# Performance work log

Measured on AMD Instinct MI355X. Metric: run time of the kernel, lower is better.

Reference implementation:

```python
import jax, jax.numpy as jnp
import numpy as np

B = 65536
IN_F = 512
OUT_F = 256
NUM_GROUPS = 8
EPS = 1e-5


def setup_inputs() -> dict:
    key = jax.random.key(0)
    ks = jax.random.split(key, 6)
    return {
        "x": jax.random.normal(ks[0], (B, IN_F), dtype=jnp.float32),
        "weight": jax.random.normal(ks[1], (OUT_F, IN_F), dtype=jnp.float32) * 0.05,
        "bias_linear": jax.random.normal(ks[2], (OUT_F,), dtype=jnp.float32) * 0.05,
        "weight_gn": jax.random.normal(ks[3], (OUT_F,), dtype=jnp.float32),
        "bias_gn": jax.random.normal(ks[4], (OUT_F,), dtype=jnp.float32),
        "bias": jax.random.normal(ks[5], (1, OUT_F, 1, 1), dtype=jnp.float32),
    }


def reference(x, weight, bias_linear, weight_gn, bias_gn, bias):
    # Linear: (B, IN_F) @ (IN_F, OUT_F) + bias -> (B, OUT_F)
    h = jnp.einsum("bi,oi->bo", x, weight) + bias_linear
    # GroupNorm over channel dim (dim=1) with NUM_GROUPS groups
    g = h.reshape(B, NUM_GROUPS, OUT_F // NUM_GROUPS)
    mean = jnp.mean(g, axis=2, keepdims=True)
    var = jnp.mean(jnp.square(g - mean), axis=2, keepdims=True)
    gn = ((g - mean) * jax.lax.rsqrt(var + EPS)).reshape(B, OUT_F)
    gn = gn * weight_gn + bias_gn
    # Min over channels, keepdim -> (B, 1)
    min_vals = jnp.min(gn, axis=1, keepdims=True)
    # torch broadcasting: (B,1) + (1,256,1,1) -> (1,256,B,1)
    result = min_vals + bias
    return result
```

## Files before the change

kernel.cpp:

```cpp
#include <hip/hip_runtime.h>
#include <hip/hip_bf16.h>

#define B_ROWS 65536
#define K_DIM  512
#define N_DIM  256
#define EPS    1e-5f
#define MTILE  32
#define NBLK   1024
#define STRIDE 520

using short8  = __attribute__((ext_vector_type(8))) short;
using floatx4 = __attribute__((ext_vector_type(4))) float;

__device__ __forceinline__ unsigned short f2bf(float f) {
    unsigned u = __builtin_bit_cast(unsigned, f);
    u += 0x7FFFu + ((u >> 16) & 1u);
    return (unsigned short)(u >> 16);
}

__global__ __launch_bounds__(64) void pack_w(const float* __restrict__ W,
                                             unsigned short* __restrict__ P) {
    int b    = blockIdx.x;
    int nt   = b >> 4, kk = b & 15;
    int lane = threadIdx.x;
    int l15  = lane & 15, quad = lane >> 4;
    const float* src = W + (size_t)(nt * 16 + l15) * K_DIM + kk * 32 + quad * 8;
    short8 v;
#pragma unroll
    for (int j = 0; j < 8; ++j) v[j] = (short)f2bf(src[j]);
    *(short8*)(P + ((size_t)(nt * 16 + kk) * 64 + lane) * 8) = v;
}

__global__ __launch_bounds__(512, 2) void fused_persistent(
    const float* __restrict__ X, const unsigned short* __restrict__ P,
    const float* __restrict__ bias_lin, const float* __restrict__ wgn,
    const float* __restrict__ bgn, const float* __restrict__ bias,
    float* __restrict__ out)
{
    __shared__ unsigned short Ash[MTILE * STRIDE];
    __shared__ float sm_min[8][MTILE];
    __shared__ float m_sh[MTILE];

    const int tid  = threadIdx.x;
    const int wave = tid >> 6, lane = tid & 63;
    const int l15  = lane & 15, quad = lane >> 4;

    short8 bfr[2][16];
#pragma unroll
    for (int ct = 0; ct < 2; ++ct)
#pragma unroll
        for (int kkg = 0; kkg < 16; ++kkg) {
            int nt = 2 * wave + ct;
            bfr[ct][kkg] = *(const short8*)(P + (((size_t)nt * 16 + kkg) * 64 + lane) * 8);
        }

    float bl[2], wg[2], bg[2];
#pragma unroll
    for (int ct = 0; ct < 2; ++ct) {
        int col = wave * 32 + ct * 16 + l15;
        bl[ct] = bias_lin[col]; wg[ct] = wgn[col]; bg[ct] = bgn[col];
    }
    float bias_r[4];
#pragma unroll
    for (int pass = 0; pass < 4; ++pass) bias_r[pass] = bias[pass * 64 + (tid >> 3)];

    const int r0 = tid >> 7;
    const int c4 = (tid & 127) * 4;

    const int tiles = B_ROWS / MTILE;
    int t = blockIdx.x;

    float4 xq[8];
#pragma unroll
    for (int p = 0; p < 8; ++p)
        xq[p] = *(const float4*)(X + (size_t)(t * MTILE + r0 + 4 * p) * K_DIM + c4);

    for (; t < tiles; t += NBLK) {
#pragma unroll
        for (int p = 0; p < 8; ++p) {
            ushort4 h;
            h.x = f2bf(xq[p].x); h.y = f2bf(xq[p].y);
            h.z = f2bf(xq[p].z); h.w = f2bf(xq[p].w);
            *(ushort4*)(&Ash[(r0 + 4 * p) * STRIDE + c4]) = h;
        }
        __syncthreads();

        int tn = t + NBLK;
        if (tn < tiles) {
#pragma unroll
            for (int p = 0; p < 8; ++p)
                xq[p] = *(const float4*)(X + (size_t)(tn * MTILE + r0 + 4 * p) * K_DIM + c4);
        }

        floatx4 acc[2][2] = {};
#pragma unroll
        for (int kk = 0; kk < 16; ++kk) {
            short8 a0 = *(const short8*)&Ash[(l15)      * STRIDE + kk * 32 + quad * 8];
            short8 a1 = *(const short8*)&Ash[(16 + l15) * STRIDE + kk * 32 + quad * 8];
            acc[0][0] = __builtin_amdgcn_mfma_f32_16x16x32_bf16(a0, bfr[0][kk], acc[0][0], 0, 0, 0);
            acc[0][1] = __builtin_amdgcn_mfma_f32_16x16x32_bf16(a0, bfr[1][kk], acc[0][1], 0, 0, 0);
            acc[1][0] = __builtin_amdgcn_mfma_f32_16x16x32_bf16(a1, bfr[0][kk], acc[1][0], 0, 0, 0);
            acc[1][1] = __builtin_amdgcn_mfma_f32_16x16x32_bf16(a1, bfr[1][kk], acc[1][1], 0, 0, 0);
        }

#pragma unroll
        for (int rt = 0; rt < 2; ++rt) {
#pragma unroll
            for (int reg = 0; reg < 4; ++reg) {
                float va = acc[rt][0][reg] + bl[0];
                float vb = acc[rt][1][reg] + bl[1];
                float s = va + vb, ss = va * va + vb * vb;
#pragma unroll
                for (int m = 1; m < 16; m <<= 1) {
                    s  += __shfl_xor(s, m);
                    ss += __shfl_xor(ss, m);
                }
                float mean = s * (1.0f / 32.0f);
                float var  = ss * (1.0f / 32.0f) - mean * mean;
                float inv  = rsqrtf(var + EPS);
                float ga = (va - mean) * inv * wg[0] + bg[0];
                float gb = (vb - mean) * inv * wg[1] + bg[1];
                float mn = fminf(ga, gb);
#pragma unroll
                for (int m = 1; m < 16; m <<= 1) mn = fminf(mn, __shfl_xor(mn, m));
                if (l15 == 0) sm_min[wave][rt * 16 + quad * 4 + reg] = mn;
            }
        }
        __syncthreads();
        if (tid < MTILE) {
            float m0 = sm_min[0][tid];
#pragma unroll
            for (int w = 1; w < 8; ++w) m0 = fminf(m0, sm_min[w][tid]);
            m_sh[tid] = m0;
        }
        __syncthreads();

        float4 mv = *(const float4*)&m_sh[(tid & 7) * 4];
#pragma unroll
        for (int pass = 0; pass < 4; ++pass) {
            int c = pass * 64 + (tid >> 3);
            float bc = bias_r[pass];
            float4 o;
            o.x = mv.x + bc; o.y = mv.y + bc; o.z = mv.z + bc; o.w = mv.w + bc;
            *(float4*)(out + (size_t)c * B_ROWS + t * MTILE + (tid & 7) * 4) = o;
        }
    }
}

extern "C" void kernel_launch(void* const* d_in, const int* in_sizes, int n_in,
                              void* d_out, int out_size, void* d_ws, size_t ws_size,
                              hipStream_t stream) {
    const float* x    = (const float*)d_in[0];
    const float* w    = (const float*)d_in[1];
    const float* bl   = (const float*)d_in[2];
    const float* wg   = (const float*)d_in[3];
    const float* bg   = (const float*)d_in[4];
    const float* bias = (const float*)d_in[5];

    unsigned short* P = (unsigned short*)d_ws;
    float* out = (float*)d_out;

    hipLaunchKernelGGL(pack_w, dim3(256), dim3(64), 0, stream, w, P);
    hipLaunchKernelGGL(fused_persistent, dim3(NBLK), dim3(512), 0, stream,
                       x, P, bl, wg, bg, bias, out);
}
```

Baseline: 246.3 us.

## Transpose MFMA operands so GroupNorm reductions stay mostly in-lane

Swaps the A/B operands of the MFMA so each lane holds four consecutive channels of one row rather than one channel of four rows. The GroupNorm sum, sum-of-squares and min reductions then run mostly inside registers and need only two cross-lane shuffles each instead of four per value. The linear bias is folded into the accumulator initialisation, and the persistent grid is halved to 512 blocks so each block covers more tiles. In exchange each lane keeps more per-channel parameter registers, and fewer blocks may expose more memory latency.

```diff
diff --git a/kernel.cpp b/kernel.cpp
--- a/kernel.cpp
+++ b/kernel.cpp
@@ -6,7 +6,7 @@
 #define N_DIM  256
 #define EPS    1e-5f
 #define MTILE  32
-#define NBLK   1024
+#define NBLK   512
 #define STRIDE 520
 
 using short8  = __attribute__((ext_vector_type(8))) short;
@@ -54,12 +54,16 @@
             bfr[ct][kkg] = *(const short8*)(P + (((size_t)nt * 16 + kkg) * 64 + lane) * 8);
         }
 
-    float bl[2], wg[2], bg[2];
+    float blr[2][4], wgr[2][4], bgr[2][4];
 #pragma unroll
-    for (int ct = 0; ct < 2; ++ct) {
-        int col = wave * 32 + ct * 16 + l15;
-        bl[ct] = bias_lin[col]; wg[ct] = wgn[col]; bg[ct] = bgn[col];
-    }
+    for (int ct = 0; ct < 2; ++ct)
+#pragma unroll
+        for (int reg = 0; reg < 4; ++reg) {
+            int c = wave * 32 + ct * 16 + quad * 4 + reg;
+            blr[ct][reg] = bias_lin[c];
+            wgr[ct][reg] = wgn[c];
+            bgr[ct][reg] = bgn[c];
+        }
     float bias_r[4];
 #pragma unroll
     for (int pass = 0; pass < 4; ++pass) bias_r[pass] = bias[pass * 64 + (tid >> 3)];
@@ -92,39 +96,52 @@
                 xq[p] = *(const float4*)(X + (size_t)(tn * MTILE + r0 + 4 * p) * K_DIM + c4);
         }
 
-        floatx4 acc[2][2] = {};
+        floatx4 acc[2][2];
+#pragma unroll
+        for (int rt = 0; rt < 2; ++rt)
+#pragma unroll
+            for (int ct = 0; ct < 2; ++ct)
+#pragma unroll
+                for (int reg = 0; reg < 4; ++reg)
+                    acc[rt][ct][reg] = blr[ct][reg];
 #pragma unroll
         for (int kk = 0; kk < 16; ++kk) {
             short8 a0 = *(const short8*)&Ash[(l15)      * STRIDE + kk * 32 + quad * 8];
             short8 a1 = *(const short8*)&Ash[(16 + l15) * STRIDE + kk * 32 + quad * 8];
-            acc[0][0] = __builtin_amdgcn_mfma_f32_16x16x32_bf16(a0, bfr[0][kk], acc[0][0], 0, 0, 0);
-            acc[0][1] = __builtin_amdgcn_mfma_f32_16x16x32_bf16(a0, bfr[1][kk], acc[0][1], 0, 0, 0);
-            acc[1][0] = __builtin_amdgcn_mfma_f32_16x16x32_bf16(a1, bfr[0][kk], acc[1][0], 0, 0, 0);
-            acc[1][1] = __builtin_amdgcn_mfma_f32_16x16x32_bf16(a1, bfr[1][kk], acc[1][1], 0, 0, 0);
+            acc[0][0] = __builtin_amdgcn_mfma_f32_16x16x32_bf16(bfr[0][kk], a0, acc[0][0], 0, 0, 0);
+            acc[0][1] = __builtin_amdgcn_mfma_f32_16x16x32_bf16(bfr[1][kk], a0, acc[0][1], 0, 0, 0);
+            acc[1][0] = __builtin_amdgcn_mfma_f32_16x16x32_bf16(bfr[0][kk], a1, acc[1][0], 0, 0, 0);
+            acc[1][1] = __builtin_amdgcn_mfma_f32_16x16x32_bf16(bfr[1][kk], a1, acc[1][1], 0, 0, 0);
         }
 
 #pragma unroll
         for (int rt = 0; rt < 2; ++rt) {
+            float s = 0.f, ss = 0.f;
 #pragma unroll
-            for (int reg = 0; reg < 4; ++reg) {
-                float va = acc[rt][0][reg] + bl[0];
-                float vb = acc[rt][1][reg] + bl[1];
-                float s = va + vb, ss = va * va + vb * vb;
+            for (int ct = 0; ct < 2; ++ct)
 #pragma unroll
-                for (int m = 1; m < 16; m <<= 1) {
-                    s  += __shfl_xor(s, m);
-                    ss += __shfl_xor(ss, m);
+                for (int reg = 0; reg < 4; ++reg) {
+                    float v = acc[rt][ct][reg];
+                    s += v; ss = fmaf(v, v, ss);
                 }
-                float mean = s * (1.0f / 32.0f);
-                float var  = ss * (1.0f / 32.0f) - mean * mean;
-                float inv  = rsqrtf(var + EPS);
-                float ga = (va - mean) * inv * wg[0] + bg[0];
-                float gb = (vb - mean) * inv * wg[1] + bg[1];
-                float mn = fminf(ga, gb);
+            s  += __shfl_xor(s, 16);  s  += __shfl_xor(s, 32);
+            ss += __shfl_xor(ss, 16); ss += __shfl_xor(ss, 32);
+            float mean = s * (1.0f / 32.0f);
+            float var  = ss * (1.0f / 32.0f) - mean * mean;
+            float inv  = rsqrtf(var + EPS);
+            float mi   = mean * inv;
+            float mn   = 1e30f;
 #pragma unroll
-                for (int m = 1; m < 16; m <<= 1) mn = fminf(mn, __shfl_xor(mn, m));
-                if (l15 == 0) sm_min[wave][rt * 16 + quad * 4 + reg] = mn;
-            }
+            for (int ct = 0; ct < 2; ++ct)
+#pragma unroll
+                for (int reg = 0; reg < 4; ++reg) {
+                    float tnorm = fmaf(acc[rt][ct][reg], inv, -mi);
+                    float g = fmaf(tnorm, wgr[ct][reg], bgr[ct][reg]);
+                    mn = fminf(mn, g);
+                }
+            mn = fminf(mn, __shfl_xor(mn, 16));
+            mn = fminf(mn, __shfl_xor(mn, 32));
+            if (quad == 0) sm_min[wave][rt * 16 + l15] = mn;
         }
         __syncthreads();
         if (tid < MTILE) {
```

Result: faster. 232.6 us (-5.6%).
